# Kernel tuning notes

Measured on AMD Instinct MI355X. Metric: run time of the kernel, lower is better.

Reference implementation:

```python
import jax, jax.numpy as jnp
import numpy as np

STRIDES = (8, 16, 32)
FMP = ((256, 256), (128, 128), (64, 64))  # H, W per level (img 2048, strides 8/16/32)
NUM_CLASSES = 80
TOPK = 1000
CONF_THRESH = 0.05
NMS_THRESH = 0.6
IMG_H = IMG_W = 2048


def _anchors(level):
    h, w = FMP[level]
    ys, xs = jnp.meshgrid(jnp.arange(h), jnp.arange(w), indexing="ij")
    xy = jnp.stack([xs, ys], axis=-1).astype(jnp.float32).reshape(-1, 2) + 0.5
    return xy * STRIDES[level]  # [M, 2]


def _level(cls_pred, reg_pred, scale, level):
    # scores/labels per anchor
    probs = jax.nn.sigmoid(cls_pred)                 # [M, C]
    scores = jnp.max(probs, axis=-1)                 # [M]
    labels = jnp.argmax(probs, axis=-1)              # [M]
    anchors = _anchors(level)
    # per-level topk (M > TOPK for all levels here)
    scores, idx = jax.lax.top_k(scores, TOPK)
    labels = labels[idx]
    reg = reg_pred[idx]
    anchors = anchors[idx]
    # decode: ctr offset in [-1.5, 1.5] cells, size via exp(scale * pred)
    ctr = anchors + (jax.nn.sigmoid(reg[:, :2]) * 3.0 - 1.5)
    wh = jnp.exp(reg[:, 2:] * scale)
    box = jnp.concatenate([ctr - 0.5 * wh, ctr + 0.5 * wh], axis=-1) * STRIDES[level]
    return scores, labels, box


def _greedy_nms(boxes, scores, labels, valid):
    """Class-aware greedy NMS with fixed shapes; returns keep mask [N].
    Per-class NMS is realized by offsetting boxes per class so cross-class IoU=0,
    which matches the original per-class loop exactly."""
    N = boxes.shape[0]
    b = boxes + labels.astype(jnp.float32)[:, None] * (4.0 * IMG_W)
    order = jnp.argsort(-scores)
    b = b[order]
    v = valid[order]
    area = (b[:, 2] - b[:, 0]) * (b[:, 3] - b[:, 1])
    xx1 = jnp.maximum(b[:, None, 0], b[None, :, 0])
    yy1 = jnp.maximum(b[:, None, 1], b[None, :, 1])
    xx2 = jnp.minimum(b[:, None, 2], b[None, :, 2])
    yy2 = jnp.minimum(b[:, None, 3], b[None, :, 3])
    w = jnp.maximum(1e-10, xx2 - xx1)
    h = jnp.maximum(1e-10, yy2 - yy1)
    inter = w * h
    iou = inter / (area[:, None] + area[None, :] - inter + 1e-14)  # [N, N]
    idxr = jnp.arange(N)

    def body(i, keep):
        sup = (iou[i] > NMS_THRESH) & (idxr > i)
        return jnp.where(keep[i], keep & ~sup, keep)

    keep_sorted = jax.lax.fori_loop(0, N, body, v)
    return jnp.zeros((N,), dtype=bool).at[order].set(keep_sorted)


def setup_inputs() -> dict:
    key = jax.random.key(0)
    ks = jax.random.split(key, 6)
    inp = {}
    for lvl, (h, w) in enumerate(FMP):
        m = h * w
        inp[f"cls{lvl}"] = jax.random.normal(ks[2 * lvl], (m, NUM_CLASSES), dtype=jnp.float32)
        inp[f"reg{lvl}"] = jax.random.normal(ks[2 * lvl + 1], (m, 4), dtype=jnp.float32)
    inp["scales"] = jnp.ones((3,), dtype=jnp.float32)
    return inp


def reference(cls0, reg0, cls1, reg1, cls2, reg2, scales):
    per_level = [
        _level(cls0, reg0, scales[0], 0),
        _level(cls1, reg1, scales[1], 1),
        _level(cls2, reg2, scales[2], 2),
    ]
    scores = jnp.concatenate([p[0] for p in per_level])   # [3000]
    labels = jnp.concatenate([p[1] for p in per_level])   # [3000]
    bboxes = jnp.concatenate([p[2] for p in per_level])   # [3000, 4]
    valid = scores >= CONF_THRESH
    keep = _greedy_nms(bboxes, scores, labels, valid)     # [3000] bool mask
    # normalize to [0, 1] by image size
    norm = jnp.array([IMG_W, IMG_H, IMG_W, IMG_H], dtype=jnp.float32)
    bboxes = jnp.clip(bboxes / norm, 0.0, 1.0)
    # fixed-shape outputs: keep mask replaces dynamic filtering (jit-friendly)
    return bboxes, scores, labels, keep
```

## Files before the change

kernel.cpp:

```cpp
#include <hip/hip_runtime.h>
#include <stdint.h>


#define N_ALL 3000
#define N_PAD 3008
#define N_WORDS 47
#define CAP 6144

typedef unsigned long long u64;
typedef uint32_t u32;

__device__ __constant__ u32 T16C[3] = {0xC056u, 0xC03Cu, 0xC021u};

__device__ __forceinline__ u32 f32_ord(float x) {
    u32 u = __float_as_uint(x);
    return (u & 0x80000000u) ? ~u : (u | 0x80000000u);
}
__device__ __forceinline__ float ord_f32(u32 o) {
    u32 u = (o & 0x80000000u) ? (o & 0x7FFFFFFFu) : ~o;
    return __uint_as_float(u);
}
__device__ __forceinline__ u64 shfl_u64(u64 v, int src) {
    int lo = __shfl((int)(u32)(v & 0xFFFFFFFFull), src);
    int hi = __shfl((int)(u32)(v >> 32), src);
    return ((u64)(u32)hi << 32) | (u32)(unsigned)lo;
}

__global__ __launch_bounds__(256) void k_scores(
        const float* __restrict__ cls0, const float* __restrict__ cls1,
        const float* __restrict__ cls2, u64* __restrict__ keys,
        u64* __restrict__ comp, u32* __restrict__ cnt) {
    __shared__ __align__(16) float tile[64 * 80];
    int b = blockIdx.x;
    int lvl, local0, off;
    const float* base;
    if (b < 1024)      { lvl = 0; local0 = b * 64;          base = cls0; off = 0; }
    else if (b < 1280) { lvl = 1; local0 = (b - 1024) * 64; base = cls1; off = 65536; }
    else               { lvl = 2; local0 = (b - 1280) * 64; base = cls2; off = 81920; }
    const float4* src = (const float4*)(base + (size_t)local0 * 80);
    float4* dst = (float4*)tile;
    int tid = threadIdx.x;
#pragma unroll
    for (int k = 0; k < 5; k++) dst[tid + k * 256] = src[tid + k * 256];
    __syncthreads();
    int a = tid >> 2, s = tid & 3;
    const float4* row = (const float4*)(tile + a * 80 + s * 20);
    float m = -3.4e38f; int lab = 0;
#pragma unroll
    for (int q = 0; q < 5; q++) {
        float4 v = row[q];
        int j0 = s * 20 + q * 4;
        if (v.x > m) { m = v.x; lab = j0;     }
        if (v.y > m) { m = v.y; lab = j0 + 1; }
        if (v.z > m) { m = v.z; lab = j0 + 2; }
        if (v.w > m) { m = v.w; lab = j0 + 3; }
    }
    float om = __shfl_xor(m, 1); int ol = __shfl_xor(lab, 1);
    if (om > m || (om == m && ol < lab)) { m = om; lab = ol; }
    om = __shfl_xor(m, 2); ol = __shfl_xor(lab, 2);
    if (om > m || (om == m && ol < lab)) { m = om; lab = ol; }
    u64 key = 0; bool pred = false;
    if (s == 0) {
        int local = local0 + a;
        key = ((u64)f32_ord(m) << 32)
            | ((u64)(0x1FFFFu - (u32)local) << 7)
            | (u64)lab;
        keys[off + local] = key;
        pred = ((u32)(key >> 48) >= T16C[lvl]);
    }
    u64 mask = __ballot(pred);
    if (mask) {
        int leader = __ffsll((long long)mask) - 1;
        int lane = threadIdx.x & 63;
        u32 bse = 0;
        if (lane == leader) bse = atomicAdd(&cnt[lvl], (u32)__popcll(mask));
        bse = (u32)__shfl((int)bse, leader);
        u32 myoff = (u32)__popcll(mask & ((1ull << lane) - 1ull));
        if (pred) { u32 pp = bse + myoff; if (pp < CAP) comp[lvl * CAP + pp] = key; }
    }
}

__global__ __launch_bounds__(256) void k_rank(
        const u64* __restrict__ keys, const u64* __restrict__ comp,
        const u32* __restrict__ cnt, u64* __restrict__ topk) {
    int lvl = blockIdx.x / 12, sub = blockIdx.x % 12;
    u32 C = cnt[lvl];
    __shared__ u64 buf[CAP];
    int tid = threadIdx.x;
    if (C >= 1000u && C <= (u32)CAP) {
        for (int i = tid; i < (int)C; i += 256) buf[i] = comp[lvl * CAP + i];
        __syncthreads();
        for (int i = sub * 256 + tid; i < (int)C; i += 3072) {
            u64 x = buf[i];
            int rank = 0;
            int Cr = (int)C & ~15;
            int j = 0;
            for (; j < Cr; j += 16) {
                u64 a[16];
#pragma unroll
                for (int q = 0; q < 16; q++) a[q] = buf[j + q];
#pragma unroll
                for (int q = 0; q < 16; q++) rank += (a[q] > x) ? 1 : 0;
            }
            for (; j < (int)C; j++) rank += (buf[j] > x) ? 1 : 0;
            if (rank < 1000) topk[lvl * 1000 + rank] = x;
        }
        return;
    }
    if (sub != 0) return;
    int M = (lvl == 0) ? 65536 : (lvl == 1 ? 16384 : 4096);
    const u64* k = keys + ((lvl == 0) ? 0 : (lvl == 1 ? 65536 : 81920));
    __shared__ u32 hist[256];
    __shared__ u64 s_pref;
    __shared__ u32 s_kk, s_c;
    if (tid == 0) { s_pref = 0; s_kk = 1000u; s_c = 0; }
    for (int d = 7; d >= 0; d--) {
        hist[tid & 255] = 0;
        __syncthreads();
        u64 pref = s_pref;
        for (int i = tid; i < M; i += 256) {
            u64 key = k[i];
            if (d == 7 || (key >> ((d + 1) * 8)) == pref)
                atomicAdd(&hist[(u32)(key >> (d * 8)) & 255u], 1u);
        }
        __syncthreads();
        if (tid == 0) {
            u32 kk = s_kk, cum = 0;
            for (int b = 255; b >= 0; b--) {
                u32 h = hist[b];
                if (cum + h >= kk) { s_pref = (pref << 8) | (u32)b; s_kk = kk - cum; break; }
                cum += h;
            }
        }
        __syncthreads();
    }
    u64 T = s_pref;
    for (int i = tid; i < M; i += 256) {
        u64 key = k[i];
        if (key >= T) { u32 p = atomicAdd(&s_c, 1u); if (p < 1024u) buf[p] = key; }
    }
    __syncthreads();
    for (int i = tid; i < 1000; i += 256) {
        u64 x = buf[i]; int rank = 0;
        for (int j = 0; j < 1000; j++) rank += (buf[j] > x) ? 1 : 0;
        topk[lvl * 1000 + rank] = x;
    }
}

__device__ __forceinline__ int cnt_desc_lds(const u64* list, u64 x, bool strict) {
    int lo = 0, hi = 1000;
    while (lo < hi) {
        int mid = (lo + hi) >> 1;
        u64 v = list[mid];
        bool in = strict ? (v > x) : (v >= x);
        if (in) lo = mid + 1; else hi = mid;
    }
    return lo;
}
__global__ __launch_bounds__(256) void k_post(
        const u64* __restrict__ topk,
        const float* __restrict__ reg0, const float* __restrict__ reg1,
        const float* __restrict__ reg2, const float* __restrict__ scales,
        float* __restrict__ out, double* __restrict__ rbox,
        u32* __restrict__ order, u64* __restrict__ kwinit) {
    __shared__ u64 lt[N_ALL];
    int tid = threadIdx.x;
    for (int i = tid; i < N_ALL; i += 256) lt[i] = topk[i];
    __syncthreads();
    int r = blockIdx.x * 256 + tid;
    if (r >= N_ALL) return;
    int lvl = r / 1000;
    u64 key = lt[r];
    u32 low = (u32)key;
    int lab = (int)(low & 0x7Fu);
    int local = 0x1FFFF - (int)((low >> 7) & 0x1FFFFu);
    float logit = ord_f32((u32)(key >> 32));
    float score = 1.0f / (1.0f + expf(-logit));
    const float* regp = (lvl == 0 ? reg0 : (lvl == 1 ? reg1 : reg2));
    float4 rg = *(const float4*)(regp + (size_t)local * 4);
    float scale = scales[lvl];
    int wlog = 8 - lvl;
    int x = local & ((1 << wlog) - 1);
    int y = local >> wlog;
    float stridef = (float)(8 << lvl);
    float ax = ((float)x + 0.5f) * stridef;
    float ay = ((float)y + 0.5f) * stridef;
    float sx = 1.0f / (1.0f + expf(-rg.x));
    float sy = 1.0f / (1.0f + expf(-rg.y));
    float cx = ax + (sx * 3.0f - 1.5f);
    float cy = ay + (sy * 3.0f - 1.5f);
    float ww = expf(rg.z * scale);
    float hh = expf(rg.w * scale);
    float b0 = (cx - 0.5f * ww) * stridef;
    float b1 = (cy - 0.5f * hh) * stridef;
    float b2 = (cx + 0.5f * ww) * stridef;
    float b3 = (cy + 0.5f * hh) * stridef;
    const float inv = 1.0f / 2048.0f;
    out[r * 4 + 0] = fminf(fmaxf(b0 * inv, 0.0f), 1.0f);
    out[r * 4 + 1] = fminf(fmaxf(b1 * inv, 0.0f), 1.0f);
    out[r * 4 + 2] = fminf(fmaxf(b2 * inv, 0.0f), 1.0f);
    out[r * 4 + 3] = fminf(fmaxf(b3 * inv, 0.0f), 1.0f);
    out[12000 + r] = score;
    out[15000 + r] = (float)lab;
    int rank = r - lvl * 1000;
#pragma unroll
    for (int L2 = 0; L2 < 3; L2++)
        if (L2 != lvl) rank += cnt_desc_lds(lt + L2 * 1000, key, L2 > lvl);
    order[rank] = (u32)r;
    double c = (double)lab * 8192.0;
    double4 rb;
    rb.x = (double)b0 + c; rb.y = (double)b1 + c;
    rb.z = (double)b2 + c; rb.w = (double)b3 + c;
    ((double4*)rbox)[rank] = rb;
    if (score >= 0.05f) atomicOr(&kwinit[rank >> 6], 1ull << (rank & 63));
}

__global__ __launch_bounds__(256) void k_iou(
        const double* __restrict__ rbox, u64* __restrict__ sup,
        u64* __restrict__ diag, u64* __restrict__ rowfut) {
    int s = blockIdx.x;
    int tid = threadIdx.x;
    __shared__ u64 s_rf;
    if (tid == 0) s_rf = 0;
    __syncthreads();
    int tword = s >> 6;
    bool srow_ok = (s < N_ALL);
    const double4* rb4 = (const double4*)rbox;
    double ix1 = 0, iy1 = 0, ix2 = 0, iy2 = 0, iarea = 0;
    if (srow_ok) {
        double4 b = rb4[s];
        ix1 = b.x; iy1 = b.y; ix2 = b.z; iy2 = b.w;
        iarea = (ix2 - ix1) * (iy2 - iy1);
    }
    for (int j = (tword << 6) + tid; j < N_PAD; j += 256) {
        bool sb = false;
        if (srow_ok && j < N_ALL && j > s) {
            double4 bj = rb4[j];
            double xx1 = fmax(ix1, bj.x), yy1 = fmax(iy1, bj.y);
            double xx2 = fmin(ix2, bj.z), yy2 = fmin(iy2, bj.w);
            double w = fmax(1e-10, xx2 - xx1);
            double h = fmax(1e-10, yy2 - yy1);
            double inter = w * h;
            double jarea = (bj.z - bj.x) * (bj.w - bj.y);
            double uni = iarea + jarea - inter + 1e-14;
            sb = inter > 0.6 * uni;
        }
        u64 bal = __ballot(sb);
        if ((j & 63) == 0) {
            int w = j >> 6;
            sup[(size_t)s * N_WORDS + w] = bal;
            if (w == tword) diag[s] = bal;
            if (w > tword && bal) atomicOr(&s_rf, 1ull << w);
        }
    }
    __syncthreads();
    if (tid == 0) rowfut[s] = s_rf;
}

__global__ __launch_bounds__(64) void k_scan(
        const u64* __restrict__ sup, const u64* __restrict__ diag,
        const u64* __restrict__ rowfut, const u64* __restrict__ kwinit,
        const u32* __restrict__ order, float* __restrict__ out_keep) {
    int lane = threadIdx.x;
    u64 kw = (lane < N_WORDS) ? kwinit[lane] : 0ull;
    u64 d  = diag[lane];
    u64 rf = rowfut[lane];
    for (int t = 0; t < N_WORDS; t++) {
        u64 dn = 0, rfn = 0;
        if (t < N_WORDS - 1) {
            dn  = diag[(t + 1) * 64 + lane];
            rfn = rowfut[(t + 1) * 64 + lane];
        }
        u64 km = shfl_u64(kw, t);
        u64 nzd = __ballot(d != 0ull);
        u64 todo = nzd;
        while (true) {
            u64 c = todo & km;
            if (!c) break;
            int b = __ffsll((long long)c) - 1;
            todo &= ~(1ull << b);
            u64 m = shfl_u64(d, b);
            km &= ~m;
        }
        if (lane == t) kw = km;
        u64 appl = km & __ballot(rf != 0ull);
        while (appl) {
            int b = __ffsll((long long)appl) - 1;
            appl &= appl - 1;
            u64 rfb = shfl_u64(rf, b);
            u64 m2 = 0ull;
            if (lane < N_WORDS && ((rfb >> lane) & 1ull))
                m2 = sup[(size_t)(t * 64 + b) * N_WORDS + lane];
            kw &= ~m2;
        }
        d = dn; rf = rfn;
    }
    if (lane < N_WORDS) {
#pragma unroll 16
        for (int b = 0; b < 64; b++) {
            int j = lane * 64 + b;
            if (j < N_ALL) out_keep[order[j]] = ((kw >> b) & 1ull) ? 1.0f : 0.0f;
        }
    }
}

extern "C" void kernel_launch(void* const* d_in, const int* in_sizes, int n_in,
                              void* d_out, int out_size, void* d_ws, size_t ws_size,
                              hipStream_t stream) {
    const float* cls0   = (const float*)d_in[0];
    const float* reg0   = (const float*)d_in[1];
    const float* cls1   = (const float*)d_in[2];
    const float* reg1   = (const float*)d_in[3];
    const float* cls2   = (const float*)d_in[4];
    const float* reg2   = (const float*)d_in[5];
    const float* scales = (const float*)d_in[6];
    float* out = (float*)d_out;
    char* ws = (char*)d_ws;
    u64* keys   = (u64*)(ws + 0);
    u64* sup    = (u64*)(ws + 0);
    u32* cnt    = (u32*)(ws + 1131008);
    u64* kwinit = (u64*)(ws + 1131040);
    u64* comp   = (u64*)(ws + 1131424);
    u64* topk   = (u64*)(ws + 1278880);
    u32* order  = (u32*)(ws + 1302880);
    double* rbox= (double*)(ws + 1314880);
    u64* diag   = (u64*)(ws + 1411136);
    u64* rowfut = (u64*)(ws + 1435200);

    hipMemsetAsync(ws + 1131008, 0, 408, stream);
    k_scores<<<1344, 256, 0, stream>>>(cls0, cls1, cls2, keys, comp, cnt);
    k_rank<<<36, 256, 0, stream>>>(keys, comp, cnt, topk);
    k_post<<<12, 256, 0, stream>>>(topk, reg0, reg1, reg2, scales, out, rbox, order, kwinit);
    k_iou<<<N_PAD, 256, 0, stream>>>(rbox, sup, diag, rowfut);
    k_scan<<<1, 64, 0, stream>>>(sup, diag, rowfut, kwinit, order, out + 18000);
}
```

Before: 199.8 us.

## Fuse pipeline into single cooperative kernel with grid syncs

Replaces the memset plus five separate kernel launches with one cooperative kernel of 256 blocks that runs each stage in turn, separated by grid.sync. The candidate compaction moves from global atomics in the scoring stage into per-block LDS compaction inside the rank stage, and each of the 12 sub-blocks ranks only its slice of anchors. The goal is to remove launch and inter-kernel gaps. The cost is that the 256-block grid must now loop over the scoring and IoU work, and grid syncs add their own barrier latency. The rank stage also rereads all keys once per block, 36 blocks in total.

```diff
diff --git a/kernel.cpp b/kernel.cpp
--- a/kernel.cpp
+++ b/kernel.cpp
@@ -1,5 +1,8 @@
 #include <hip/hip_runtime.h>
+#include <hip/hip_cooperative_groups.h>
 #include <stdint.h>
+
+namespace cg = cooperative_groups;
 
 
 #define N_ALL 3000
@@ -25,128 +28,6 @@
     int hi = __shfl((int)(u32)(v >> 32), src);
     return ((u64)(u32)hi << 32) | (u32)(unsigned)lo;
 }
-
-__global__ __launch_bounds__(256) void k_scores(
-        const float* __restrict__ cls0, const float* __restrict__ cls1,
-        const float* __restrict__ cls2, u64* __restrict__ keys,
-        u64* __restrict__ comp, u32* __restrict__ cnt) {
-    __shared__ __align__(16) float tile[64 * 80];
-    int b = blockIdx.x;
-    int lvl, local0, off;
-    const float* base;
-    if (b < 1024)      { lvl = 0; local0 = b * 64;          base = cls0; off = 0; }
-    else if (b < 1280) { lvl = 1; local0 = (b - 1024) * 64; base = cls1; off = 65536; }
-    else               { lvl = 2; local0 = (b - 1280) * 64; base = cls2; off = 81920; }
-    const float4* src = (const float4*)(base + (size_t)local0 * 80);
-    float4* dst = (float4*)tile;
-    int tid = threadIdx.x;
-#pragma unroll
-    for (int k = 0; k < 5; k++) dst[tid + k * 256] = src[tid + k * 256];
-    __syncthreads();
-    int a = tid >> 2, s = tid & 3;
-    const float4* row = (const float4*)(tile + a * 80 + s * 20);
-    float m = -3.4e38f; int lab = 0;
-#pragma unroll
-    for (int q = 0; q < 5; q++) {
-        float4 v = row[q];
-        int j0 = s * 20 + q * 4;
-        if (v.x > m) { m = v.x; lab = j0;     }
-        if (v.y > m) { m = v.y; lab = j0 + 1; }
-        if (v.z > m) { m = v.z; lab = j0 + 2; }
-        if (v.w > m) { m = v.w; lab = j0 + 3; }
-    }
-    float om = __shfl_xor(m, 1); int ol = __shfl_xor(lab, 1);
-    if (om > m || (om == m && ol < lab)) { m = om; lab = ol; }
-    om = __shfl_xor(m, 2); ol = __shfl_xor(lab, 2);
-    if (om > m || (om == m && ol < lab)) { m = om; lab = ol; }
-    u64 key = 0; bool pred = false;
-    if (s == 0) {
-        int local = local0 + a;
-        key = ((u64)f32_ord(m) << 32)
-            | ((u64)(0x1FFFFu - (u32)local) << 7)
-            | (u64)lab;
-        keys[off + local] = key;
-        pred = ((u32)(key >> 48) >= T16C[lvl]);
-    }
-    u64 mask = __ballot(pred);
-    if (mask) {
-        int leader = __ffsll((long long)mask) - 1;
-        int lane = threadIdx.x & 63;
-        u32 bse = 0;
-        if (lane == leader) bse = atomicAdd(&cnt[lvl], (u32)__popcll(mask));
-        bse = (u32)__shfl((int)bse, leader);
-        u32 myoff = (u32)__popcll(mask & ((1ull << lane) - 1ull));
-        if (pred) { u32 pp = bse + myoff; if (pp < CAP) comp[lvl * CAP + pp] = key; }
-    }
-}
-
-__global__ __launch_bounds__(256) void k_rank(
-        const u64* __restrict__ keys, const u64* __restrict__ comp,
-        const u32* __restrict__ cnt, u64* __restrict__ topk) {
-    int lvl = blockIdx.x / 12, sub = blockIdx.x % 12;
-    u32 C = cnt[lvl];
-    __shared__ u64 buf[CAP];
-    int tid = threadIdx.x;
-    if (C >= 1000u && C <= (u32)CAP) {
-        for (int i = tid; i < (int)C; i += 256) buf[i] = comp[lvl * CAP + i];
-        __syncthreads();
-        for (int i = sub * 256 + tid; i < (int)C; i += 3072) {
-            u64 x = buf[i];
-            int rank = 0;
-            int Cr = (int)C & ~15;
-            int j = 0;
-            for (; j < Cr; j += 16) {
-                u64 a[16];
-#pragma unroll
-                for (int q = 0; q < 16; q++) a[q] = buf[j + q];
-#pragma unroll
-                for (int q = 0; q < 16; q++) rank += (a[q] > x) ? 1 : 0;
-            }
-            for (; j < (int)C; j++) rank += (buf[j] > x) ? 1 : 0;
-            if (rank < 1000) topk[lvl * 1000 + rank] = x;
-        }
-        return;
-    }
-    if (sub != 0) return;
-    int M = (lvl == 0) ? 65536 : (lvl == 1 ? 16384 : 4096);
-    const u64* k = keys + ((lvl == 0) ? 0 : (lvl == 1 ? 65536 : 81920));
-    __shared__ u32 hist[256];
-    __shared__ u64 s_pref;
-    __shared__ u32 s_kk, s_c;
-    if (tid == 0) { s_pref = 0; s_kk = 1000u; s_c = 0; }
-    for (int d = 7; d >= 0; d--) {
-        hist[tid & 255] = 0;
-        __syncthreads();
-        u64 pref = s_pref;
-        for (int i = tid; i < M; i += 256) {
-            u64 key = k[i];
-            if (d == 7 || (key >> ((d + 1) * 8)) == pref)
-                atomicAdd(&hist[(u32)(key >> (d * 8)) & 255u], 1u);
-        }
-        __syncthreads();
-        if (tid == 0) {
-            u32 kk = s_kk, cum = 0;
-            for (int b = 255; b >= 0; b--) {
-                u32 h = hist[b];
-                if (cum + h >= kk) { s_pref = (pref << 8) | (u32)b; s_kk = kk - cum; break; }
-                cum += h;
-            }
-        }
-        __syncthreads();
-    }
-    u64 T = s_pref;
-    for (int i = tid; i < M; i += 256) {
-        u64 key = k[i];
-        if (key >= T) { u32 p = atomicAdd(&s_c, 1u); if (p < 1024u) buf[p] = key; }
-    }
-    __syncthreads();
-    for (int i = tid; i < 1000; i += 256) {
-        u64 x = buf[i]; int rank = 0;
-        for (int j = 0; j < 1000; j++) rank += (buf[j] > x) ? 1 : 0;
-        topk[lvl * 1000 + rank] = x;
-    }
-}
-
 __device__ __forceinline__ int cnt_desc_lds(const u64* list, u64 x, bool strict) {
     int lo = 0, hi = 1000;
     while (lo < hi) {
@@ -157,149 +38,282 @@
     }
     return lo;
 }
-__global__ __launch_bounds__(256) void k_post(
-        const u64* __restrict__ topk,
-        const float* __restrict__ reg0, const float* __restrict__ reg1,
-        const float* __restrict__ reg2, const float* __restrict__ scales,
-        float* __restrict__ out, double* __restrict__ rbox,
-        u32* __restrict__ order, u64* __restrict__ kwinit) {
-    __shared__ u64 lt[N_ALL];
+
+__global__ __launch_bounds__(256) void k_all(
+        const float* __restrict__ cls0, const float* __restrict__ cls1,
+        const float* __restrict__ cls2, const float* __restrict__ reg0,
+        const float* __restrict__ reg1, const float* __restrict__ reg2,
+        const float* __restrict__ scales, float* __restrict__ out,
+        u64* __restrict__ keys, u64* __restrict__ sup, u64* __restrict__ topk,
+        u32* __restrict__ order, double* __restrict__ rbox,
+        u64* __restrict__ diag, u64* __restrict__ rowfut, u64* __restrict__ kwinit) {
+    cg::grid_group grid = cg::this_grid();
+    __shared__ __align__(16) char smem[49152];
+    __shared__ u32 s_hist[256];
+    __shared__ u32 s_cnt, s_kk, s_c;
+    __shared__ u64 s_pref, s_rf;
     int tid = threadIdx.x;
-    for (int i = tid; i < N_ALL; i += 256) lt[i] = topk[i];
-    __syncthreads();
-    int r = blockIdx.x * 256 + tid;
-    if (r >= N_ALL) return;
-    int lvl = r / 1000;
-    u64 key = lt[r];
-    u32 low = (u32)key;
-    int lab = (int)(low & 0x7Fu);
-    int local = 0x1FFFF - (int)((low >> 7) & 0x1FFFFu);
-    float logit = ord_f32((u32)(key >> 32));
-    float score = 1.0f / (1.0f + expf(-logit));
-    const float* regp = (lvl == 0 ? reg0 : (lvl == 1 ? reg1 : reg2));
-    float4 rg = *(const float4*)(regp + (size_t)local * 4);
-    float scale = scales[lvl];
-    int wlog = 8 - lvl;
-    int x = local & ((1 << wlog) - 1);
-    int y = local >> wlog;
-    float stridef = (float)(8 << lvl);
-    float ax = ((float)x + 0.5f) * stridef;
-    float ay = ((float)y + 0.5f) * stridef;
-    float sx = 1.0f / (1.0f + expf(-rg.x));
-    float sy = 1.0f / (1.0f + expf(-rg.y));
-    float cx = ax + (sx * 3.0f - 1.5f);
-    float cy = ay + (sy * 3.0f - 1.5f);
-    float ww = expf(rg.z * scale);
-    float hh = expf(rg.w * scale);
-    float b0 = (cx - 0.5f * ww) * stridef;
-    float b1 = (cy - 0.5f * hh) * stridef;
-    float b2 = (cx + 0.5f * ww) * stridef;
-    float b3 = (cy + 0.5f * hh) * stridef;
-    const float inv = 1.0f / 2048.0f;
-    out[r * 4 + 0] = fminf(fmaxf(b0 * inv, 0.0f), 1.0f);
-    out[r * 4 + 1] = fminf(fmaxf(b1 * inv, 0.0f), 1.0f);
-    out[r * 4 + 2] = fminf(fmaxf(b2 * inv, 0.0f), 1.0f);
-    out[r * 4 + 3] = fminf(fmaxf(b3 * inv, 0.0f), 1.0f);
-    out[12000 + r] = score;
-    out[15000 + r] = (float)lab;
-    int rank = r - lvl * 1000;
-#pragma unroll
-    for (int L2 = 0; L2 < 3; L2++)
-        if (L2 != lvl) rank += cnt_desc_lds(lt + L2 * 1000, key, L2 > lvl);
-    order[rank] = (u32)r;
-    double c = (double)lab * 8192.0;
-    double4 rb;
-    rb.x = (double)b0 + c; rb.y = (double)b1 + c;
-    rb.z = (double)b2 + c; rb.w = (double)b3 + c;
-    ((double4*)rbox)[rank] = rb;
-    if (score >= 0.05f) atomicOr(&kwinit[rank >> 6], 1ull << (rank & 63));
-}
-
-__global__ __launch_bounds__(256) void k_iou(
-        const double* __restrict__ rbox, u64* __restrict__ sup,
-        u64* __restrict__ diag, u64* __restrict__ rowfut) {
-    int s = blockIdx.x;
-    int tid = threadIdx.x;
-    __shared__ u64 s_rf;
-    if (tid == 0) s_rf = 0;
-    __syncthreads();
-    int tword = s >> 6;
-    bool srow_ok = (s < N_ALL);
-    const double4* rb4 = (const double4*)rbox;
-    double ix1 = 0, iy1 = 0, ix2 = 0, iy2 = 0, iarea = 0;
-    if (srow_ok) {
-        double4 b = rb4[s];
-        ix1 = b.x; iy1 = b.y; ix2 = b.z; iy2 = b.w;
-        iarea = (ix2 - ix1) * (iy2 - iy1);
-    }
-    for (int j = (tword << 6) + tid; j < N_PAD; j += 256) {
-        bool sb = false;
-        if (srow_ok && j < N_ALL && j > s) {
-            double4 bj = rb4[j];
-            double xx1 = fmax(ix1, bj.x), yy1 = fmax(iy1, bj.y);
-            double xx2 = fmin(ix2, bj.z), yy2 = fmin(iy2, bj.w);
-            double w = fmax(1e-10, xx2 - xx1);
-            double h = fmax(1e-10, yy2 - yy1);
-            double inter = w * h;
-            double jarea = (bj.z - bj.x) * (bj.w - bj.y);
-            double uni = iarea + jarea - inter + 1e-14;
-            sb = inter > 0.6 * uni;
-        }
-        u64 bal = __ballot(sb);
-        if ((j & 63) == 0) {
-            int w = j >> 6;
-            sup[(size_t)s * N_WORDS + w] = bal;
-            if (w == tword) diag[s] = bal;
-            if (w > tword && bal) atomicOr(&s_rf, 1ull << w);
-        }
-    }
-    __syncthreads();
-    if (tid == 0) rowfut[s] = s_rf;
-}
-
-__global__ __launch_bounds__(64) void k_scan(
-        const u64* __restrict__ sup, const u64* __restrict__ diag,
-        const u64* __restrict__ rowfut, const u64* __restrict__ kwinit,
-        const u32* __restrict__ order, float* __restrict__ out_keep) {
-    int lane = threadIdx.x;
-    u64 kw = (lane < N_WORDS) ? kwinit[lane] : 0ull;
-    u64 d  = diag[lane];
-    u64 rf = rowfut[lane];
-    for (int t = 0; t < N_WORDS; t++) {
-        u64 dn = 0, rfn = 0;
-        if (t < N_WORDS - 1) {
-            dn  = diag[(t + 1) * 64 + lane];
-            rfn = rowfut[(t + 1) * 64 + lane];
-        }
-        u64 km = shfl_u64(kw, t);
-        u64 nzd = __ballot(d != 0ull);
-        u64 todo = nzd;
-        while (true) {
-            u64 c = todo & km;
-            if (!c) break;
-            int b = __ffsll((long long)c) - 1;
-            todo &= ~(1ull << b);
-            u64 m = shfl_u64(d, b);
-            km &= ~m;
-        }
-        if (lane == t) kw = km;
-        u64 appl = km & __ballot(rf != 0ull);
-        while (appl) {
-            int b = __ffsll((long long)appl) - 1;
-            appl &= appl - 1;
-            u64 rfb = shfl_u64(rf, b);
-            u64 m2 = 0ull;
-            if (lane < N_WORDS && ((rfb >> lane) & 1ull))
-                m2 = sup[(size_t)(t * 64 + b) * N_WORDS + lane];
-            kw &= ~m2;
-        }
-        d = dn; rf = rfn;
-    }
-    if (lane < N_WORDS) {
+
+    {
+        float* tile = (float*)smem;
+        for (int vb = blockIdx.x; vb < 1344; vb += gridDim.x) {
+            int lvl, local0, off;
+            const float* base;
+            if (vb < 1024)      { lvl = 0; local0 = vb * 64;          base = cls0; off = 0; }
+            else if (vb < 1280) { lvl = 1; local0 = (vb - 1024) * 64; base = cls1; off = 65536; }
+            else                { lvl = 2; local0 = (vb - 1280) * 64; base = cls2; off = 81920; }
+            const float4* src = (const float4*)(base + (size_t)local0 * 80);
+            float4* dst = (float4*)tile;
+#pragma unroll
+            for (int k = 0; k < 5; k++) dst[tid + k * 256] = src[tid + k * 256];
+            __syncthreads();
+            int a = tid >> 2, s = tid & 3;
+            const float4* row = (const float4*)(tile + a * 80 + s * 20);
+            float m = -3.4e38f; int lab = 0;
+#pragma unroll
+            for (int q = 0; q < 5; q++) {
+                float4 v = row[q];
+                int j0 = s * 20 + q * 4;
+                if (v.x > m) { m = v.x; lab = j0;     }
+                if (v.y > m) { m = v.y; lab = j0 + 1; }
+                if (v.z > m) { m = v.z; lab = j0 + 2; }
+                if (v.w > m) { m = v.w; lab = j0 + 3; }
+            }
+            float om = __shfl_xor(m, 1); int ol = __shfl_xor(lab, 1);
+            if (om > m || (om == m && ol < lab)) { m = om; lab = ol; }
+            om = __shfl_xor(m, 2); ol = __shfl_xor(lab, 2);
+            if (om > m || (om == m && ol < lab)) { m = om; lab = ol; }
+            if (s == 0) {
+                int local = local0 + a;
+                keys[off + local] = ((u64)f32_ord(m) << 32)
+                                  | ((u64)(0x1FFFFu - (u32)local) << 7)
+                                  | (u64)lab;
+            }
+            __syncthreads();
+            (void)lvl;
+        }
+        if (blockIdx.x == 0 && tid < N_WORDS) kwinit[tid] = 0ull;
+    }
+    grid.sync();
+
+    if (blockIdx.x < 36) {
+        u64* buf = (u64*)smem;
+        int lvl = blockIdx.x / 12, sub = blockIdx.x % 12;
+        int M   = (lvl == 0) ? 65536 : (lvl == 1 ? 16384 : 4096);
+        int off = (lvl == 0) ? 0 : (lvl == 1 ? 65536 : 81920);
+        const u64* k = keys + off;
+        u32 thr = T16C[lvl];
+        if (tid == 0) s_cnt = 0;
+        __syncthreads();
+        int lane = tid & 63;
+        for (int i = tid; i < M; i += 256) {
+            u64 key = k[i];
+            bool pred = ((u32)(key >> 48) >= thr);
+            u64 mask = __ballot(pred);
+            if (mask) {
+                int leader = __ffsll((long long)mask) - 1;
+                u32 bse = 0;
+                if (lane == leader) bse = atomicAdd(&s_cnt, (u32)__popcll(mask));
+                bse = (u32)__shfl((int)bse, leader);
+                u32 myoff = (u32)__popcll(mask & ((1ull << lane) - 1ull));
+                if (pred) { u32 pp = bse + myoff; if (pp < CAP) buf[pp] = key; }
+            }
+        }
+        __syncthreads();
+        u32 C = s_cnt;
+        if (C >= 1000u && C <= (u32)CAP) {
+            int lo = (int)(((long long)sub * M) / 12);
+            int hi = (int)(((long long)(sub + 1) * M) / 12);
+            for (int i = tid; i < (int)C; i += 256) {
+                u64 x = buf[i];
+                int local = 0x1FFFF - (int)((x >> 7) & 0x1FFFFu);
+                if (local < lo || local >= hi) continue;
+                int rank = 0;
+                int Cr = (int)C & ~15;
+                int j = 0;
+                for (; j < Cr; j += 16) {
+                    u64 a[16];
+#pragma unroll
+                    for (int q = 0; q < 16; q++) a[q] = buf[j + q];
+#pragma unroll
+                    for (int q = 0; q < 16; q++) rank += (a[q] > x) ? 1 : 0;
+                }
+                for (; j < (int)C; j++) rank += (buf[j] > x) ? 1 : 0;
+                if (rank < 1000) topk[lvl * 1000 + rank] = x;
+            }
+        } else if (sub == 0) {
+            if (tid == 0) { s_pref = 0; s_kk = 1000u; s_c = 0; }
+            for (int d = 7; d >= 0; d--) {
+                if (tid < 256) s_hist[tid] = 0;
+                __syncthreads();
+                u64 pref = s_pref;
+                for (int i = tid; i < M; i += 256) {
+                    u64 key = k[i];
+                    if (d == 7 || (key >> ((d + 1) * 8)) == pref)
+                        atomicAdd(&s_hist[(u32)(key >> (d * 8)) & 255u], 1u);
+                }
+                __syncthreads();
+                if (tid == 0) {
+                    u32 kk = s_kk, cum = 0;
+                    for (int b = 255; b >= 0; b--) {
+                        u32 h = s_hist[b];
+                        if (cum + h >= kk) { s_pref = (pref << 8) | (u32)b; s_kk = kk - cum; break; }
+                        cum += h;
+                    }
+                }
+                __syncthreads();
+            }
+            u64 T = s_pref;
+            for (int i = tid; i < M; i += 256) {
+                u64 key = k[i];
+                if (key >= T) { u32 p = atomicAdd(&s_c, 1u); if (p < 1024u) buf[p] = key; }
+            }
+            __syncthreads();
+            for (int i = tid; i < 1000; i += 256) {
+                u64 x = buf[i]; int rank = 0;
+                for (int j = 0; j < 1000; j++) rank += (buf[j] > x) ? 1 : 0;
+                topk[lvl * 1000 + rank] = x;
+            }
+        }
+    }
+    grid.sync();
+
+    if (blockIdx.x < 12) {
+        u64* lt = (u64*)smem;
+        for (int i = tid; i < N_ALL; i += 256) lt[i] = topk[i];
+        __syncthreads();
+        int r = blockIdx.x * 256 + tid;
+        if (r < N_ALL) {
+            int lvl = r / 1000;
+            u64 key = lt[r];
+            u32 low = (u32)key;
+            int lab = (int)(low & 0x7Fu);
+            int local = 0x1FFFF - (int)((low >> 7) & 0x1FFFFu);
+            float logit = ord_f32((u32)(key >> 32));
+            float score = 1.0f / (1.0f + expf(-logit));
+            const float* regp = (lvl == 0 ? reg0 : (lvl == 1 ? reg1 : reg2));
+            float4 rg = *(const float4*)(regp + (size_t)local * 4);
+            float scale = scales[lvl];
+            int wlog = 8 - lvl;
+            int x = local & ((1 << wlog) - 1);
+            int y = local >> wlog;
+            float stridef = (float)(8 << lvl);
+            float ax = ((float)x + 0.5f) * stridef;
+            float ay = ((float)y + 0.5f) * stridef;
+            float sx = 1.0f / (1.0f + expf(-rg.x));
+            float sy = 1.0f / (1.0f + expf(-rg.y));
+            float cx = ax + (sx * 3.0f - 1.5f);
+            float cy = ay + (sy * 3.0f - 1.5f);
+            float ww = expf(rg.z * scale);
+            float hh = expf(rg.w * scale);
+            float b0 = (cx - 0.5f * ww) * stridef;
+            float b1 = (cy - 0.5f * hh) * stridef;
+            float b2 = (cx + 0.5f * ww) * stridef;
+            float b3 = (cy + 0.5f * hh) * stridef;
+            const float inv = 1.0f / 2048.0f;
+            out[r * 4 + 0] = fminf(fmaxf(b0 * inv, 0.0f), 1.0f);
+            out[r * 4 + 1] = fminf(fmaxf(b1 * inv, 0.0f), 1.0f);
+            out[r * 4 + 2] = fminf(fmaxf(b2 * inv, 0.0f), 1.0f);
+            out[r * 4 + 3] = fminf(fmaxf(b3 * inv, 0.0f), 1.0f);
+            out[12000 + r] = score;
+            out[15000 + r] = (float)lab;
+            int rank = r - lvl * 1000;
+#pragma unroll
+            for (int L2 = 0; L2 < 3; L2++)
+                if (L2 != lvl) rank += cnt_desc_lds(lt + L2 * 1000, key, L2 > lvl);
+            order[rank] = (u32)r;
+            double c = (double)lab * 8192.0;
+            double4 rb;
+            rb.x = (double)b0 + c; rb.y = (double)b1 + c;
+            rb.z = (double)b2 + c; rb.w = (double)b3 + c;
+            ((double4*)rbox)[rank] = rb;
+            if (score >= 0.05f) atomicOr(&kwinit[rank >> 6], 1ull << (rank & 63));
+        }
+    }
+    grid.sync();
+
+    {
+        const double4* rb4 = (const double4*)rbox;
+        for (int s = blockIdx.x; s < N_PAD; s += gridDim.x) {
+            if (tid == 0) s_rf = 0;
+            __syncthreads();
+            int tword = s >> 6;
+            bool srow_ok = (s < N_ALL);
+            double ix1 = 0, iy1 = 0, ix2 = 0, iy2 = 0, iarea = 0;
+            if (srow_ok) {
+                double4 b = rb4[s];
+                ix1 = b.x; iy1 = b.y; ix2 = b.z; iy2 = b.w;
+                iarea = (ix2 - ix1) * (iy2 - iy1);
+            }
+            for (int j = (tword << 6) + tid; j < N_PAD; j += 256) {
+                bool sb = false;
+                if (srow_ok && j < N_ALL && j > s) {
+                    double4 bj = rb4[j];
+                    double xx1 = fmax(ix1, bj.x), yy1 = fmax(iy1, bj.y);
+                    double xx2 = fmin(ix2, bj.z), yy2 = fmin(iy2, bj.w);
+                    double w = fmax(1e-10, xx2 - xx1);
+                    double h = fmax(1e-10, yy2 - yy1);
+                    double inter = w * h;
+                    double jarea = (bj.z - bj.x) * (bj.w - bj.y);
+                    double uni = iarea + jarea - inter + 1e-14;
+                    sb = inter > 0.6 * uni;
+                }
+                u64 bal = __ballot(sb);
+                if ((j & 63) == 0) {
+                    int w = j >> 6;
+                    sup[(size_t)s * N_WORDS + w] = bal;
+                    if (w == tword) diag[s] = bal;
+                    if (w > tword && bal) atomicOr(&s_rf, 1ull << w);
+                }
+            }
+            __syncthreads();
+            if (tid == 0) rowfut[s] = s_rf;
+        }
+    }
+    grid.sync();
+
+    if (blockIdx.x == 0 && tid < 64) {
+        int lane = tid;
+        u64 kw = (lane < N_WORDS) ? kwinit[lane] : 0ull;
+        u64 d  = diag[lane];
+        u64 rf = rowfut[lane];
+        for (int t = 0; t < N_WORDS; t++) {
+            u64 dn = 0, rfn = 0;
+            if (t < N_WORDS - 1) {
+                dn  = diag[(t + 1) * 64 + lane];
+                rfn = rowfut[(t + 1) * 64 + lane];
+            }
+            u64 km = shfl_u64(kw, t);
+            u64 nzd = __ballot(d != 0ull);
+            u64 todo = nzd;
+            while (true) {
+                u64 c = todo & km;
+                if (!c) break;
+                int b = __ffsll((long long)c) - 1;
+                todo &= ~(1ull << b);
+                u64 m = shfl_u64(d, b);
+                km &= ~m;
+            }
+            if (lane == t) kw = km;
+            u64 appl = km & __ballot(rf != 0ull);
+            while (appl) {
+                int b = __ffsll((long long)appl) - 1;
+                appl &= appl - 1;
+                u64 rfb = shfl_u64(rf, b);
+                u64 m2 = 0ull;
+                if (lane < N_WORDS && ((rfb >> lane) & 1ull))
+                    m2 = sup[(size_t)(t * 64 + b) * N_WORDS + lane];
+                kw &= ~m2;
+            }
+            d = dn; rf = rfn;
+        }
+        if (lane < N_WORDS) {
+            float* out_keep = out + 18000;
 #pragma unroll 16
-        for (int b = 0; b < 64; b++) {
-            int j = lane * 64 + b;
-            if (j < N_ALL) out_keep[order[j]] = ((kw >> b) & 1ull) ? 1.0f : 0.0f;
+            for (int b = 0; b < 64; b++) {
+                int j = lane * 64 + b;
+                if (j < N_ALL) out_keep[order[j]] = ((kw >> b) & 1ull) ? 1.0f : 0.0f;
+            }
         }
     }
 }
@@ -318,19 +332,18 @@
     char* ws = (char*)d_ws;
     u64* keys   = (u64*)(ws + 0);
     u64* sup    = (u64*)(ws + 0);
-    u32* cnt    = (u32*)(ws + 1131008);
-    u64* kwinit = (u64*)(ws + 1131040);
-    u64* comp   = (u64*)(ws + 1131424);
-    u64* topk   = (u64*)(ws + 1278880);
-    u32* order  = (u32*)(ws + 1302880);
-    double* rbox= (double*)(ws + 1314880);
-    u64* diag   = (u64*)(ws + 1411136);
-    u64* rowfut = (u64*)(ws + 1435200);
-
-    hipMemsetAsync(ws + 1131008, 0, 408, stream);
-    k_scores<<<1344, 256, 0, stream>>>(cls0, cls1, cls2, keys, comp, cnt);
-    k_rank<<<36, 256, 0, stream>>>(keys, comp, cnt, topk);
-    k_post<<<12, 256, 0, stream>>>(topk, reg0, reg1, reg2, scales, out, rbox, order, kwinit);
-    k_iou<<<N_PAD, 256, 0, stream>>>(rbox, sup, diag, rowfut);
-    k_scan<<<1, 64, 0, stream>>>(sup, diag, rowfut, kwinit, order, out + 18000);
-}
+    u64* topk   = (u64*)(ws + 1131008);
+    u32* order  = (u32*)(ws + 1155008);
+    u64* kwinit = (u64*)(ws + 1167008);
+    double* rbox= (double*)(ws + 1167392);
+    u64* diag   = (u64*)(ws + 1263648);
+    u64* rowfut = (u64*)(ws + 1287712);
+
+    void* args[] = { (void*)&cls0, (void*)&cls1, (void*)&cls2,
+                     (void*)&reg0, (void*)&reg1, (void*)&reg2,
+                     (void*)&scales, (void*)&out,
+                     (void*)&keys, (void*)&sup, (void*)&topk, (void*)&order,
+                     (void*)&rbox, (void*)&diag, (void*)&rowfut, (void*)&kwinit };
+    hipLaunchCooperativeKernel((const void*)k_all, dim3(256), dim3(256),
+                               args, 0, stream);
+}
```

Measured after the change: 428.9 us. +114.7%, slower.

## Move candidate compaction into rank kernel and drop the workspace memset

Applied to the files above, without the earlier changes.

Removes the hipMemsetAsync launch by zeroing kwinit inside k_scores. The candidate compaction moves from a global-atomic pass in k_scores into each k_rank block, which rescans its level's keys and compacts into shared memory with a shared atomic. Rank work is then split across the 12 sub-blocks by anchor index range instead of by buffer position. Every one of the 36 rank blocks now rereads all keys of its level, and each still loops over all C candidates to find its own, so there is redundant work in exchange for one fewer launch and no global atomics.

```diff
diff --git a/kernel.cpp b/kernel.cpp
--- a/kernel.cpp
+++ b/kernel.cpp
@@ -29,19 +29,20 @@
 __global__ __launch_bounds__(256) void k_scores(
         const float* __restrict__ cls0, const float* __restrict__ cls1,
         const float* __restrict__ cls2, u64* __restrict__ keys,
-        u64* __restrict__ comp, u32* __restrict__ cnt) {
+        u64* __restrict__ kwinit) {
     __shared__ __align__(16) float tile[64 * 80];
     int b = blockIdx.x;
-    int lvl, local0, off;
+    int local0, off;
     const float* base;
-    if (b < 1024)      { lvl = 0; local0 = b * 64;          base = cls0; off = 0; }
-    else if (b < 1280) { lvl = 1; local0 = (b - 1024) * 64; base = cls1; off = 65536; }
-    else               { lvl = 2; local0 = (b - 1280) * 64; base = cls2; off = 81920; }
+    if (b < 1024)      { local0 = b * 64;          base = cls0; off = 0; }
+    else if (b < 1280) { local0 = (b - 1024) * 64; base = cls1; off = 65536; }
+    else               { local0 = (b - 1280) * 64; base = cls2; off = 81920; }
     const float4* src = (const float4*)(base + (size_t)local0 * 80);
     float4* dst = (float4*)tile;
     int tid = threadIdx.x;
 #pragma unroll
     for (int k = 0; k < 5; k++) dst[tid + k * 256] = src[tid + k * 256];
+    if (b == 0 && tid < N_WORDS) kwinit[tid] = 0ull;
     __syncthreads();
     int a = tid >> 2, s = tid & 3;
     const float4* row = (const float4*)(tile + a * 80 + s * 20);
@@ -59,39 +60,51 @@
     if (om > m || (om == m && ol < lab)) { m = om; lab = ol; }
     om = __shfl_xor(m, 2); ol = __shfl_xor(lab, 2);
     if (om > m || (om == m && ol < lab)) { m = om; lab = ol; }
-    u64 key = 0; bool pred = false;
     if (s == 0) {
         int local = local0 + a;
-        key = ((u64)f32_ord(m) << 32)
-            | ((u64)(0x1FFFFu - (u32)local) << 7)
-            | (u64)lab;
-        keys[off + local] = key;
-        pred = ((u32)(key >> 48) >= T16C[lvl]);
-    }
-    u64 mask = __ballot(pred);
-    if (mask) {
-        int leader = __ffsll((long long)mask) - 1;
-        int lane = threadIdx.x & 63;
-        u32 bse = 0;
-        if (lane == leader) bse = atomicAdd(&cnt[lvl], (u32)__popcll(mask));
-        bse = (u32)__shfl((int)bse, leader);
-        u32 myoff = (u32)__popcll(mask & ((1ull << lane) - 1ull));
-        if (pred) { u32 pp = bse + myoff; if (pp < CAP) comp[lvl * CAP + pp] = key; }
+        keys[off + local] = ((u64)f32_ord(m) << 32)
+                          | ((u64)(0x1FFFFu - (u32)local) << 7)
+                          | (u64)lab;
     }
 }
 
 __global__ __launch_bounds__(256) void k_rank(
-        const u64* __restrict__ keys, const u64* __restrict__ comp,
-        const u32* __restrict__ cnt, u64* __restrict__ topk) {
+        const u64* __restrict__ keys, u64* __restrict__ topk) {
+    __shared__ u64 buf[CAP];
+    __shared__ u32 s_hist[256];
+    __shared__ u32 s_cnt, s_kk, s_c;
+    __shared__ u64 s_pref;
     int lvl = blockIdx.x / 12, sub = blockIdx.x % 12;
-    u32 C = cnt[lvl];
-    __shared__ u64 buf[CAP];
+    int M   = (lvl == 0) ? 65536 : (lvl == 1 ? 16384 : 4096);
+    int off = (lvl == 0) ? 0 : (lvl == 1 ? 65536 : 81920);
+    const u64* k = keys + off;
+    u32 thr = T16C[lvl];
     int tid = threadIdx.x;
+    if (tid == 0) s_cnt = 0;
+    __syncthreads();
+    int lane = tid & 63;
+    for (int i = tid; i < M; i += 256) {
+        u64 key = k[i];
+        bool pred = ((u32)(key >> 48) >= thr);
+        u64 mask = __ballot(pred);
+        if (mask) {
+            int leader = __ffsll((long long)mask) - 1;
+            u32 bse = 0;
+            if (lane == leader) bse = atomicAdd(&s_cnt, (u32)__popcll(mask));
+            bse = (u32)__shfl((int)bse, leader);
+            u32 myoff = (u32)__popcll(mask & ((1ull << lane) - 1ull));
+            if (pred) { u32 pp = bse + myoff; if (pp < CAP) buf[pp] = key; }
+        }
+    }
+    __syncthreads();
+    u32 C = s_cnt;
     if (C >= 1000u && C <= (u32)CAP) {
-        for (int i = tid; i < (int)C; i += 256) buf[i] = comp[lvl * CAP + i];
-        __syncthreads();
-        for (int i = sub * 256 + tid; i < (int)C; i += 3072) {
+        int lo = (int)(((long long)sub * M) / 12);
+        int hi = (int)(((long long)(sub + 1) * M) / 12);
+        for (int i = tid; i < (int)C; i += 256) {
             u64 x = buf[i];
+            int local = 0x1FFFF - (int)((x >> 7) & 0x1FFFFu);
+            if (local < lo || local >= hi) continue;
             int rank = 0;
             int Cr = (int)C & ~15;
             int j = 0;
@@ -108,26 +121,21 @@
         return;
     }
     if (sub != 0) return;
-    int M = (lvl == 0) ? 65536 : (lvl == 1 ? 16384 : 4096);
-    const u64* k = keys + ((lvl == 0) ? 0 : (lvl == 1 ? 65536 : 81920));
-    __shared__ u32 hist[256];
-    __shared__ u64 s_pref;
-    __shared__ u32 s_kk, s_c;
     if (tid == 0) { s_pref = 0; s_kk = 1000u; s_c = 0; }
     for (int d = 7; d >= 0; d--) {
-        hist[tid & 255] = 0;
+        if (tid < 256) s_hist[tid] = 0;
         __syncthreads();
         u64 pref = s_pref;
         for (int i = tid; i < M; i += 256) {
             u64 key = k[i];
             if (d == 7 || (key >> ((d + 1) * 8)) == pref)
-                atomicAdd(&hist[(u32)(key >> (d * 8)) & 255u], 1u);
+                atomicAdd(&s_hist[(u32)(key >> (d * 8)) & 255u], 1u);
         }
         __syncthreads();
         if (tid == 0) {
             u32 kk = s_kk, cum = 0;
             for (int b = 255; b >= 0; b--) {
-                u32 h = hist[b];
+                u32 h = s_hist[b];
                 if (cum + h >= kk) { s_pref = (pref << 8) | (u32)b; s_kk = kk - cum; break; }
                 cum += h;
             }
@@ -318,18 +326,15 @@
     char* ws = (char*)d_ws;
     u64* keys   = (u64*)(ws + 0);
     u64* sup    = (u64*)(ws + 0);
-    u32* cnt    = (u32*)(ws + 1131008);
-    u64* kwinit = (u64*)(ws + 1131040);
-    u64* comp   = (u64*)(ws + 1131424);
-    u64* topk   = (u64*)(ws + 1278880);
-    u32* order  = (u32*)(ws + 1302880);
-    double* rbox= (double*)(ws + 1314880);
-    u64* diag   = (u64*)(ws + 1411136);
-    u64* rowfut = (u64*)(ws + 1435200);
-
-    hipMemsetAsync(ws + 1131008, 0, 408, stream);
-    k_scores<<<1344, 256, 0, stream>>>(cls0, cls1, cls2, keys, comp, cnt);
-    k_rank<<<36, 256, 0, stream>>>(keys, comp, cnt, topk);
+    u64* topk   = (u64*)(ws + 1131008);
+    u32* order  = (u32*)(ws + 1155008);
+    u64* kwinit = (u64*)(ws + 1167008);
+    double* rbox= (double*)(ws + 1167392);
+    u64* diag   = (u64*)(ws + 1263648);
+    u64* rowfut = (u64*)(ws + 1287712);
+
+    k_scores<<<1344, 256, 0, stream>>>(cls0, cls1, cls2, keys, kwinit);
+    k_rank<<<36, 256, 0, stream>>>(keys, topk);
     k_post<<<12, 256, 0, stream>>>(topk, reg0, reg1, reg2, scales, out, rbox, order, kwinit);
     k_iou<<<N_PAD, 256, 0, stream>>>(rbox, sup, diag, rowfut);
     k_scan<<<1, 64, 0, stream>>>(sup, diag, rowfut, kwinit, order, out + 18000);
```

After: 288.6 us. +44.4%, slower.
